# Kernel tuning notes

Hardware: AMD Instinct MI355X
Metric: run time of the kernel (lower is better)

## Reference

```python
import jax, jax.numpy as jnp
import numpy as np

T = 32            # timesteps_count
DT = 1e-3
TAU_MEM_INV = 100.0   # norse LIFParameters default (1/1e-2)
TAU_SYN_INV = 200.0   # norse default (1/5e-3)
V_TH = 1.0
ALPHA = 100.0         # SuperSpike surrogate slope


@jax.custom_vjp
def superspike(x):
    # Heaviside forward, SuperSpike surrogate backward (norse 'super' method)
    return (x > 0).astype(x.dtype)

def _ss_fwd(x):
    return (x > 0).astype(x.dtype), x

def _ss_bwd(x, g):
    return (g / (ALPHA * jnp.abs(x) + 1.0) ** 2,)

superspike.defvjp(_ss_fwd, _ss_bwd)


def setup_inputs() -> dict:
    key = jax.random.key(0)
    k1, k2 = jax.random.split(key)
    image = jax.random.uniform(k1, (4096, 1, 28, 28), dtype=jnp.float32)
    # LILinearCell input weights, shape [out_features, in_features]
    W = jax.random.normal(k2, (10, 784), dtype=jnp.float32) * np.sqrt(2.0 / 784.0).astype(np.float32)
    return {"image": image, "W": W}


def reference(image, W):
    B = image.shape[0]
    x = image.reshape(B, -1)  # [B, 784] constant input current

    def step(carry, _):
        v_enc, v0, i0, v_out, i_out = carry
        # --- ConstantCurrentLIFEncoder (lif_current_encoder step) ---
        v_enc = v_enc + DT * TAU_MEM_INV * (-v_enc + x)
        z_enc = superspike(v_enc - V_TH)
        v_enc = v_enc - z_enc * v_enc  # reset to v_reset = 0
        # --- LIFCell (feed-forward LIF step) ---
        v_dec = v0 + DT * TAU_MEM_INV * (-v0 + i0)
        i_dec = i0 - DT * TAU_SYN_INV * i0
        z0 = superspike(v_dec - V_TH)
        v0_new = (1.0 - z0) * v_dec          # v_reset = 0
        i0_new = i_dec + z_enc
        # --- LILinearCell (leaky integrator with linear input) ---
        i_jump = i_out + z0 @ W.T            # [B, 10]
        v_out_new = v_out + DT * TAU_MEM_INV * (-v_out + i_jump)
        i_out_new = i_jump - DT * TAU_SYN_INV * i_jump
        return (v_enc, v0_new, i0_new, v_out_new, i_out_new), v_out_new

    z784 = jnp.zeros_like(x)
    z10 = jnp.zeros((B, 10), dtype=x.dtype)
    _, vs = jax.lax.scan(step, (z784, z784, z784, z10, z10), None, length=T)
    v_max = jnp.max(vs, axis=0)              # max over timesteps, [B, 10]
    return jax.nn.log_softmax(v_max, axis=1)
```

## Files before the change

### kernel.cpp

```cpp
#include <hip/hip_runtime.h>
#include <math.h>


#define N_IN   784
#define N_OUT  10
#define T_STEPS 32
#define ROW_F4 196
#define WS_ROW 2382

__global__ __launch_bounds__(256) void snn_wave_kernel(
    const float* __restrict__ image,
    const float* __restrict__ W,
    float* __restrict__ out,
    float* __restrict__ ws,
    int B)
{
    constexpr float DT_TMI  = 0.1f;
    constexpr float DEC_SYN = 0.8f;
    constexpr float V_TH    = 1.0f;
    constexpr float NEG_LOG10 = -2.30258509299404568402f;

    const int wave = threadIdx.x >> 6;
    const int lane = threadIdx.x & 63;
    const int row  = blockIdx.x * 4 + wave;
    if (row >= B) return;

    const float4* __restrict__ x4 = (const float4*)(image + (size_t)row * N_IN);

    const bool has4 = (lane < 4);
    float4 c0 = x4[lane];
    float4 c1 = x4[lane + 64];
    float4 c2 = x4[lane + 128];
    float4 c3 = has4 ? x4[lane + 192] : make_float4(0.f, 0.f, 0.f, 0.f);

    float m = fmaxf(fmaxf(fmaxf(c0.x, c0.y), fmaxf(c0.z, c0.w)),
                    fmaxf(fmaxf(c1.x, c1.y), fmaxf(c1.z, c1.w)));
    m = fmaxf(m, fmaxf(fmaxf(c2.x, c2.y), fmaxf(c2.z, c2.w)));
    m = fmaxf(m, fmaxf(fmaxf(c3.x, c3.y), fmaxf(c3.z, c3.w)));

    if (!__any(m > V_TH)) {
        if (lane < N_OUT) out[(size_t)row * N_OUT + lane] = NEG_LOG10;
        return;
    }

    float* const rb   = ws + (size_t)row * WS_ROW;
    float* const p_ve = rb;
    float* const p_v0 = rb + N_IN;
    float* const p_i0 = rb + 2 * N_IN;
    float* const p_ro = rb + 3 * N_IN;

    const float xv[16] = { c0.x, c0.y, c0.z, c0.w,  c1.x, c1.y, c1.z, c1.w,
                           c2.x, c2.y, c2.z, c2.w,  c3.x, c3.y, c3.z, c3.w };
    const int   cbase[4] = { lane, lane + 64, lane + 128, lane + 192 };
    const int   nch = has4 ? 4 : 3;

    for (int c = 0; c < nch; ++c) {
        const int j0 = 4 * cbase[c];
#pragma unroll
        for (int e = 0; e < 4; ++e) {
            p_ve[j0 + e] = 0.0f; p_v0[j0 + e] = 0.0f; p_i0[j0 + e] = 0.0f;
        }
    }
    if (lane == 0) {
#pragma unroll
        for (int o = 0; o < N_OUT; ++o) {
            p_ro[o] = 0.0f;
            p_ro[10 + o] = 0.0f;
            p_ro[20 + o] = -INFINITY;
        }
    }

    for (int t = 0; t < T_STEPS; ++t) {
        float s[N_OUT];
#pragma unroll
        for (int o = 0; o < N_OUT; ++o) s[o] = 0.0f;

        for (int c = 0; c < nch; ++c) {
            const int j0 = 4 * cbase[c];
#pragma unroll
            for (int e = 0; e < 4; ++e) {
                const int j = j0 + e;
                const float x = xv[4 * c + e];
                float ve = p_ve[j], v0 = p_v0[j], i0 = p_i0[j];
                ve += DT_TMI * (x - ve);
                const float z_enc = (ve > V_TH) ? 1.0f : 0.0f;
                ve = (ve > V_TH) ? 0.0f : ve;
                const float v_dec = v0 + DT_TMI * (i0 - v0);
                const float i_dec = DEC_SYN * i0;
                const bool  z0    = v_dec > V_TH;
                p_ve[j] = ve;
                p_v0[j] = z0 ? 0.0f : v_dec;
                p_i0[j] = i_dec + z_enc;
                if (z0) {
#pragma unroll
                    for (int o = 0; o < N_OUT; ++o) s[o] += W[o * N_IN + j];
                }
            }
        }

#pragma unroll
        for (int o = 0; o < N_OUT; ++o) {
            float v = s[o];
            v += __shfl_down(v, 32, 64);
            v += __shfl_down(v, 16, 64);
            v += __shfl_down(v,  8, 64);
            v += __shfl_down(v,  4, 64);
            v += __shfl_down(v,  2, 64);
            v += __shfl_down(v,  1, 64);
            s[o] = v;
        }

        if (lane == 0) {
#pragma unroll
            for (int o = 0; o < N_OUT; ++o) {
                const float jump = p_ro[10 + o] + s[o];
                const float v    = p_ro[o] + DT_TMI * (jump - p_ro[o]);
                p_ro[o]      = v;
                p_ro[10 + o] = DEC_SYN * jump;
                p_ro[20 + o] = fmaxf(p_ro[20 + o], v);
            }
        }
    }

    if (lane == 0) {
        float mm = -INFINITY;
#pragma unroll
        for (int o = 0; o < N_OUT; ++o) mm = fmaxf(mm, p_ro[20 + o]);
        float sum = 0.0f;
#pragma unroll
        for (int o = 0; o < N_OUT; ++o) sum += expf(p_ro[20 + o] - mm);
        const float lse = mm + logf(sum);
        float* orow = out + (size_t)row * N_OUT;
#pragma unroll
        for (int o = 0; o < N_OUT; ++o) orow[o] = p_ro[20 + o] - lse;
    }
}

extern "C" void kernel_launch(void* const* d_in, const int* in_sizes, int n_in,
                              void* d_out, int out_size, void* d_ws, size_t ws_size,
                              hipStream_t stream) {
    const float* image = (const float*)d_in[0];
    const float* W     = (const float*)d_in[1];
    float*       out   = (float*)d_out;

    const int B = in_sizes[0] / N_IN;
    const int blocks = (B + 3) / 4;
    snn_wave_kernel<<<blocks, 256, 0, stream>>>(image, W, out, (float*)d_ws, B);
}
```

Before: 61.80 us.

## Keep per-neuron SNN state in registers instead of global workspace

Moves the encoder, hidden and synaptic state of each lane's 16 neurons, and the readout state, out of a per-row global workspace and into registers, with the inner loops fully unrolled. This removes three global loads and three stores per neuron per timestep. The lane reduction switches to xor shuffles so every lane holds the sums and the readout update runs redundantly with no lane-0 branch. Input loads and the early-exit store become nontemporal. Register pressure rises, which may lower occupancy.

```diff
diff --git a/kernel.cpp b/kernel.cpp
--- a/kernel.cpp
+++ b/kernel.cpp
@@ -2,17 +2,16 @@
 #include <math.h>
 
 
-#define N_IN   784
-#define N_OUT  10
+#define N_IN    784
+#define N_OUT   10
 #define T_STEPS 32
-#define ROW_F4 196
-#define WS_ROW 2382
+
+typedef float floatx4 __attribute__((ext_vector_type(4)));
 
 __global__ __launch_bounds__(256) void snn_wave_kernel(
     const float* __restrict__ image,
     const float* __restrict__ W,
     float* __restrict__ out,
-    float* __restrict__ ws,
     int B)
 {
     constexpr float DT_TMI  = 0.1f;
@@ -25,13 +24,14 @@
     const int row  = blockIdx.x * 4 + wave;
     if (row >= B) return;
 
-    const float4* __restrict__ x4 = (const float4*)(image + (size_t)row * N_IN);
+    const floatx4* __restrict__ x4 = (const floatx4*)(image + (size_t)row * N_IN);
 
     const bool has4 = (lane < 4);
-    float4 c0 = x4[lane];
-    float4 c1 = x4[lane + 64];
-    float4 c2 = x4[lane + 128];
-    float4 c3 = has4 ? x4[lane + 192] : make_float4(0.f, 0.f, 0.f, 0.f);
+    floatx4 c0 = __builtin_nontemporal_load(x4 + lane);
+    floatx4 c1 = __builtin_nontemporal_load(x4 + lane + 64);
+    floatx4 c2 = __builtin_nontemporal_load(x4 + lane + 128);
+    floatx4 c3 = (floatx4)(0.f);
+    if (has4) c3 = __builtin_nontemporal_load(x4 + lane + 192);
 
     float m = fmaxf(fmaxf(fmaxf(c0.x, c0.y), fmaxf(c0.z, c0.w)),
                     fmaxf(fmaxf(c1.x, c1.y), fmaxf(c1.z, c1.w)));
@@ -39,58 +39,44 @@
     m = fmaxf(m, fmaxf(fmaxf(c3.x, c3.y), fmaxf(c3.z, c3.w)));
 
     if (!__any(m > V_TH)) {
-        if (lane < N_OUT) out[(size_t)row * N_OUT + lane] = NEG_LOG10;
+        if (lane < N_OUT)
+            __builtin_nontemporal_store(NEG_LOG10, out + (size_t)row * N_OUT + lane);
         return;
     }
 
-    float* const rb   = ws + (size_t)row * WS_ROW;
-    float* const p_ve = rb;
-    float* const p_v0 = rb + N_IN;
-    float* const p_i0 = rb + 2 * N_IN;
-    float* const p_ro = rb + 3 * N_IN;
+    float xv[16] = { c0.x, c0.y, c0.z, c0.w,  c1.x, c1.y, c1.z, c1.w,
+                     c2.x, c2.y, c2.z, c2.w,  c3.x, c3.y, c3.z, c3.w };
+    float ve[16], vh[16], ih[16];
+#pragma unroll
+    for (int k = 0; k < 16; ++k) { ve[k] = 0.f; vh[k] = 0.f; ih[k] = 0.f; }
 
-    const float xv[16] = { c0.x, c0.y, c0.z, c0.w,  c1.x, c1.y, c1.z, c1.w,
-                           c2.x, c2.y, c2.z, c2.w,  c3.x, c3.y, c3.z, c3.w };
-    const int   cbase[4] = { lane, lane + 64, lane + 128, lane + 192 };
-    const int   nch = has4 ? 4 : 3;
-
-    for (int c = 0; c < nch; ++c) {
-        const int j0 = 4 * cbase[c];
+    float vo[N_OUT], io[N_OUT], vmax[N_OUT];
 #pragma unroll
-        for (int e = 0; e < 4; ++e) {
-            p_ve[j0 + e] = 0.0f; p_v0[j0 + e] = 0.0f; p_i0[j0 + e] = 0.0f;
-        }
-    }
-    if (lane == 0) {
-#pragma unroll
-        for (int o = 0; o < N_OUT; ++o) {
-            p_ro[o] = 0.0f;
-            p_ro[10 + o] = 0.0f;
-            p_ro[20 + o] = -INFINITY;
-        }
-    }
+    for (int o = 0; o < N_OUT; ++o) { vo[o] = 0.f; io[o] = 0.f; vmax[o] = -INFINITY; }
 
     for (int t = 0; t < T_STEPS; ++t) {
         float s[N_OUT];
 #pragma unroll
-        for (int o = 0; o < N_OUT; ++o) s[o] = 0.0f;
+        for (int o = 0; o < N_OUT; ++o) s[o] = 0.f;
 
-        for (int c = 0; c < nch; ++c) {
-            const int j0 = 4 * cbase[c];
+#pragma unroll
+        for (int cc = 0; cc < 4; ++cc) {
+            const int gbase = (cc < 3) ? (lane + 64 * cc)
+                                       : (has4 ? (192 + lane) : 0);
 #pragma unroll
             for (int e = 0; e < 4; ++e) {
-                const int j = j0 + e;
-                const float x = xv[4 * c + e];
-                float ve = p_ve[j], v0 = p_v0[j], i0 = p_i0[j];
-                ve += DT_TMI * (x - ve);
-                const float z_enc = (ve > V_TH) ? 1.0f : 0.0f;
-                ve = (ve > V_TH) ? 0.0f : ve;
-                const float v_dec = v0 + DT_TMI * (i0 - v0);
-                const float i_dec = DEC_SYN * i0;
-                const bool  z0    = v_dec > V_TH;
-                p_ve[j] = ve;
-                p_v0[j] = z0 ? 0.0f : v_dec;
-                p_i0[j] = i_dec + z_enc;
+                const int k = 4 * cc + e;
+                const int j = 4 * gbase + e;
+                const float x = xv[k];
+                float v = ve[k];
+                v += DT_TMI * (x - v);
+                const float z_enc = (v > V_TH) ? 1.0f : 0.0f;
+                ve[k] = (v > V_TH) ? 0.0f : v;
+                const float vd = vh[k] + DT_TMI * (ih[k] - vh[k]);
+                const float id = DEC_SYN * ih[k];
+                const bool  z0 = vd > V_TH;
+                vh[k] = z0 ? 0.0f : vd;
+                ih[k] = id + z_enc;
                 if (z0) {
 #pragma unroll
                     for (int o = 0; o < N_OUT; ++o) s[o] += W[o * N_IN + j];
@@ -101,39 +87,37 @@
 #pragma unroll
         for (int o = 0; o < N_OUT; ++o) {
             float v = s[o];
-            v += __shfl_down(v, 32, 64);
-            v += __shfl_down(v, 16, 64);
-            v += __shfl_down(v,  8, 64);
-            v += __shfl_down(v,  4, 64);
-            v += __shfl_down(v,  2, 64);
-            v += __shfl_down(v,  1, 64);
+            v += __shfl_xor(v, 32, 64);
+            v += __shfl_xor(v, 16, 64);
+            v += __shfl_xor(v,  8, 64);
+            v += __shfl_xor(v,  4, 64);
+            v += __shfl_xor(v,  2, 64);
+            v += __shfl_xor(v,  1, 64);
             s[o] = v;
         }
 
-        if (lane == 0) {
 #pragma unroll
-            for (int o = 0; o < N_OUT; ++o) {
-                const float jump = p_ro[10 + o] + s[o];
-                const float v    = p_ro[o] + DT_TMI * (jump - p_ro[o]);
-                p_ro[o]      = v;
-                p_ro[10 + o] = DEC_SYN * jump;
-                p_ro[20 + o] = fmaxf(p_ro[20 + o], v);
-            }
+        for (int o = 0; o < N_OUT; ++o) {
+            const float jump = io[o] + s[o];
+            const float v    = vo[o] + DT_TMI * (jump - vo[o]);
+            vo[o]   = v;
+            io[o]   = DEC_SYN * jump;
+            vmax[o] = fmaxf(vmax[o], v);
         }
     }
 
-    if (lane == 0) {
-        float mm = -INFINITY;
+    float mm = -INFINITY;
 #pragma unroll
-        for (int o = 0; o < N_OUT; ++o) mm = fmaxf(mm, p_ro[20 + o]);
-        float sum = 0.0f;
+    for (int o = 0; o < N_OUT; ++o) mm = fmaxf(mm, vmax[o]);
+    float sum = 0.0f;
 #pragma unroll
-        for (int o = 0; o < N_OUT; ++o) sum += expf(p_ro[20 + o] - mm);
-        const float lse = mm + logf(sum);
-        float* orow = out + (size_t)row * N_OUT;
+    for (int o = 0; o < N_OUT; ++o) sum += expf(vmax[o] - mm);
+    const float lse = mm + logf(sum);
+
+    float myv = vmax[0];
 #pragma unroll
-        for (int o = 0; o < N_OUT; ++o) orow[o] = p_ro[20 + o] - lse;
-    }
+    for (int o = 1; o < N_OUT; ++o) myv = (lane == o) ? vmax[o] : myv;
+    if (lane < N_OUT) out[(size_t)row * N_OUT + lane] = myv - lse;
 }
 
 extern "C" void kernel_launch(void* const* d_in, const int* in_sizes, int n_in,
@@ -142,8 +126,9 @@
     const float* image = (const float*)d_in[0];
     const float* W     = (const float*)d_in[1];
     float*       out   = (float*)d_out;
+    (void)d_ws; (void)ws_size;
 
     const int B = in_sizes[0] / N_IN;
     const int blocks = (B + 3) / 4;
-    snn_wave_kernel<<<blocks, 256, 0, stream>>>(image, W, out, (float*)d_ws, B);
+    snn_wave_kernel<<<blocks, 256, 0, stream>>>(image, W, out, B);
 }
```

Result: no change. 63.00 us (+2.0%).
